# Optimization experiments

Hardware: AMD Instinct MI355X
Metric: run time of the kernel (lower is better)

Reference implementation:

```python
import jax, jax.numpy as jnp
from jax import lax
import numpy as np

IN_SIZE, H_SIZE, OUT_SIZE, SEAS = 48, 128, 48, 24
DILATIONS = (1, 2, 4, 8)  # cells 0-1 = DRNN group 0, cells 2-3 = DRNN group 1


def setup_inputs() -> dict:
    key = jax.random.key(0)
    ks = jax.random.split(key, 16)
    B, T = 256, 512
    inp = {
        'train': jax.random.uniform(ks[0], (B, T), jnp.float32, 0.5, 1.5),
        'val': jax.random.uniform(ks[1], (B, OUT_SIZE), jnp.float32, 0.5, 1.5),
        'test': jax.random.uniform(ks[2], (B, OUT_SIZE), jnp.float32, 0.5, 1.5),
        'init_lev_sm': jnp.array([0.5], jnp.float32),
        'init_seas_sm': jnp.array([0.5], jnp.float32),
        'init_seasonalities': jnp.full((SEAS,), 0.5, jnp.float32),
    }
    cin = [IN_SIZE, H_SIZE, H_SIZE, H_SIZE]
    k = 3
    for i in range(4):
        inp[f'w_ih{i}'] = jax.random.normal(ks[k], (4 * H_SIZE, cin[i]), jnp.float32) * 0.05; k += 1
        inp[f'w_hh{i}'] = jax.random.normal(ks[k], (4 * H_SIZE, H_SIZE), jnp.float32) * 0.05; k += 1
        inp[f'b_ih{i}'] = jnp.zeros((4 * H_SIZE,), jnp.float32)
        inp[f'b_hh{i}'] = jnp.zeros((4 * H_SIZE,), jnp.float32)
    inp['nl_w'] = jax.random.normal(ks[k], (H_SIZE, H_SIZE), jnp.float32) * 0.05; k += 1
    inp['nl_b'] = jnp.zeros((H_SIZE,), jnp.float32)
    inp['sc_w'] = jax.random.normal(ks[k], (OUT_SIZE, H_SIZE), jnp.float32) * 0.05; k += 1
    inp['sc_b'] = jnp.zeros((OUT_SIZE,), jnp.float32)
    return inp


def _lstm(x, w_ih, w_hh, b_ih, b_hh):
    # x: (T, N, C) -> (T, N, H); torch LSTM gate order i, f, g, o
    n, h = x.shape[1], w_hh.shape[1]

    def step(carry, xt):
        hp, cp = carry
        g = xt @ w_ih.T + hp @ w_hh.T + (b_ih + b_hh)
        i, f, gg, o = jnp.split(g, 4, axis=-1)
        c = jax.nn.sigmoid(f) * cp + jax.nn.sigmoid(i) * jnp.tanh(gg)
        hn = jax.nn.sigmoid(o) * jnp.tanh(c)
        return (hn, c), hn

    z = jnp.zeros((n, h), x.dtype)
    _, hs = lax.scan(step, (z, z), x)
    return hs


def _dilated_lstm(x, d, w_ih, w_hh, b_ih, b_hh):
    # DRNN dilation: fold time by d into batch, run cell, unfold
    t, b, c = x.shape
    td = -(-t // d) * d
    xp = jnp.pad(x, ((0, td - t), (0, 0), (0, 0)))
    xd = xp.reshape(td // d, d, b, c).reshape(td // d, d * b, c)
    out = _lstm(xd, w_ih, w_hh, b_ih, b_hh)
    h = out.shape[-1]
    return out.reshape(td // d, d, b, h).reshape(td, b, h)[:t]


def _series_forward(data, cells, nl_w, nl_b, sc_w, sc_b):
    # ResidualDRNN: group 0 (cells 0,1), group 1 (cells 2,3) with residual add
    x = data
    for grp in range(2):
        res = x
        for ci in (2 * grp, 2 * grp + 1):
            x = _dilated_lstm(x, DILATIONS[ci], *cells[ci])
        if grp > 0:
            x = x + res
    x = jnp.tanh(x @ nl_w.T + nl_b)
    return x @ sc_w.T + sc_b


def _esrnn(train, val, init_lev_sm, init_seas_sm, init_seasonalities, cells, nl_w, nl_b, sc_w, sc_b):
    B, T = train.shape
    lev_sm = jax.nn.sigmoid(init_lev_sm[0])
    seas_sm = jax.nn.sigmoid(init_seas_sm[0])
    s0 = jnp.exp(init_seasonalities)  # (SEAS,) shared across series
    lev0 = train[:, 0] / s0[0]  # (B,)
    # rolling buffer: at step i it holds seasonalities[i .. i+SEAS-1]
    buf0 = jnp.broadcast_to(jnp.concatenate([s0[1:], s0[:1]])[:, None], (SEAS, B))

    def step(carry, x_t):
        lev_p, buf = carry
        seas_t = buf[0]
        lev_n = lev_sm * (x_t / seas_t) + (1 - lev_sm) * lev_p
        seas_n = seas_sm * (x_t / lev_n) + (1 - seas_sm) * seas_t
        return (lev_n, jnp.concatenate([buf[1:], seas_n[None]], 0)), (lev_n, seas_n)

    _, (levs_r, seas_r) = lax.scan(step, (lev0, buf0), train[:, 1:].T)
    levs = jnp.concatenate([lev0[None], levs_r], 0).T  # (B, T)
    seas_head = jnp.broadcast_to(jnp.concatenate([s0, s0[:1]])[:, None], (SEAS + 1, B))
    seas = jnp.concatenate([seas_head, seas_r], 0).T  # (B, T+SEAS)
    if OUT_SIZE > SEAS:  # seasonality extension branch
        start = seas.shape[1] - SEAS
        seas = jnp.concatenate([seas, seas[:, start:start + OUT_SIZE - SEAS]], 1)
    W = T - IN_SIZE + 1
    Wo = T - OUT_SIZE - IN_SIZE + 1
    idx_in = jnp.arange(W)[:, None] + jnp.arange(IN_SIZE)[None, :]  # (W, IN)
    win_in = (train[:, idx_in] / seas[:, idx_in] / levs[:, IN_SIZE - 1:, None]).transpose(1, 0, 2)  # (W,B,IN)
    idx_out = jnp.arange(Wo)[:, None] + IN_SIZE + jnp.arange(OUT_SIZE)[None, :]
    win_out = (train[:, idx_out] / seas[:, idx_out] / levs[:, IN_SIZE - 1:IN_SIZE - 1 + Wo, None]).transpose(1, 0, 2)
    network_pred = _series_forward(win_in[:-OUT_SIZE], cells, nl_w, nl_b, sc_w, sc_b)  # (Wo,B,OUT)
    network_act = win_out
    net_out_all = _series_forward(win_in, cells, nl_w, nl_b, sc_w, sc_b)  # (W,B,OUT)
    hold = net_out_all[-1] * seas[:, -OUT_SIZE:] * levs[:, -1:]
    hold_out_pred = hold * (hold > 0).astype(hold.dtype)
    hold_out_act = val  # testing=False path
    hold_out_act_norm = val / seas[:, -OUT_SIZE:] / levs[:, -1:]
    return network_pred, network_act, hold_out_pred, net_out_all, hold_out_act, hold_out_act_norm


def reference(train, val, test, init_lev_sm, init_seas_sm, init_seasonalities,
              w_ih0, w_hh0, b_ih0, b_hh0, w_ih1, w_hh1, b_ih1, b_hh1,
              w_ih2, w_hh2, b_ih2, b_hh2, w_ih3, w_hh3, b_ih3, b_hh3,
              nl_w, nl_b, sc_w, sc_b):
    cells = ((w_ih0, w_hh0, b_ih0, b_hh0), (w_ih1, w_hh1, b_ih1, b_hh1),
             (w_ih2, w_hh2, b_ih2, b_hh2), (w_ih3, w_hh3, b_ih3, b_hh3))
    return _esrnn(train, val, init_lev_sm, init_seas_sm, init_seasonalities,
                  cells, nl_w, nl_b, sc_w, sc_b)
```

## Files before the change

### kernel.cpp

```cpp
#include <hip/hip_runtime.h>
#include <cstdint>
#include <cstddef>

typedef _Float16 half8 __attribute__((ext_vector_type(8)));
typedef _Float16 half4 __attribute__((ext_vector_type(4)));
typedef float floatx4 __attribute__((ext_vector_type(4)));

namespace {
constexpr int kB = 256, kT = 512, kIN = 48, kOUT = 48, kSEAS = 24, kH = 128;
constexpr int kW = kT - kIN + 1;
constexpr int kWO = kT - kOUT - kIN + 1;
constexpr int kNB = kW * kB;
constexpr int kMBLK = kNB / 16;
constexpr float kLOG2E = 1.44269504088896340736f;
}

#if __has_builtin(__builtin_amdgcn_exp2f)
#define FEXP2(x) __builtin_amdgcn_exp2f(x)
#else
#define FEXP2(x) exp2f(x)
#endif
#if __has_builtin(__builtin_amdgcn_rcpf)
#define FRCP(x) __builtin_amdgcn_rcpf(x)
#else
#define FRCP(x) (1.0f / (x))
#endif

#define LGKM_BARRIER() asm volatile("s_waitcnt lgkmcnt(0)\n\ts_barrier" ::: "memory")

__device__ __forceinline__ float fsig(float y) { return FRCP(1.0f + FEXP2(-y)); }
__device__ __forceinline__ float ftanh(float x) { return 2.0f * fsig(2.0f * kLOG2E * x) - 1.0f; }

__global__ void k_transpose(const float* __restrict__ train, float* __restrict__ trainT) {
  int t = blockIdx.x, b = threadIdx.x;
  trainT[t * kB + b] = train[b * kT + t];
}

__global__ void k_es(const float* __restrict__ trainT, const float* __restrict__ levp,
                     const float* __restrict__ seasp, const float* __restrict__ inits,
                     float* __restrict__ seas, float* __restrict__ levs) {
  __shared__ float ring[kSEAS][kB];
  int b = threadIdx.x;
  float lev_sm = fsig(levp[0] * kLOG2E);
  float seas_sm = fsig(seasp[0] * kLOG2E);
  float s00 = expf(inits[0]);
  for (int s = 0; s < kSEAS; ++s) {
    float v = expf(inits[s]);
    seas[s * kB + b] = v;
    if (s >= 1) ring[s - 1][b] = v;
  }
  ring[kSEAS - 1][b] = s00;
  seas[kSEAS * kB + b] = s00;
  float lev = trainT[b] * FRCP(s00);
  levs[b] = lev;
  int rk = 0;
  float x_nx = trainT[kB + b];
  float st_nx = ring[0][b];
  for (int k = 0; k < kT - 1; ++k) {
    float x = x_nx;
    float st = st_nx;
    if (k + 1 < kT - 1) x_nx = trainT[(k + 2) * kB + b];
    int rn = (rk + 1 == kSEAS) ? 0 : rk + 1;
    st_nx = ring[rn][b];
    float ln = lev_sm * (x * FRCP(st)) + (1.0f - lev_sm) * lev;
    float sn = seas_sm * (x * FRCP(ln)) + (1.0f - seas_sm) * st;
    ring[rk][b] = sn;
    seas[(k + kSEAS + 1) * kB + b] = sn;
    levs[(k + 1) * kB + b] = ln;
    lev = ln;
    rk = rn;
  }
  for (int j = 0; j < kOUT - kSEAS; ++j)
    seas[(kT + kSEAS + j) * kB + b] = seas[(kT + j) * kB + b];
}

__global__ void k_win_in(const float* __restrict__ trainT, const float* __restrict__ seas,
                         const float* __restrict__ levs, _Float16* __restrict__ win) {
  int w = blockIdx.x;
  int tid = threadIdx.x;
#pragma unroll
  for (int i = 0; i < 16; ++i) {
    int o = i * 256 + tid;
    int b = o >> 3;
    int j0 = (o & 7) * 8;
    half8 h;
    if (j0 < kIN) {
      float rl = FRCP(levs[(kIN - 1 + w) * kB + b]);
#pragma unroll
      for (int jj = 0; jj < 8; ++jj) {
        int j = j0 + jj;
        int t = w + j;
        float v = (j < kIN) ? trainT[t * kB + b] * FRCP(seas[t * kB + b]) * rl : 0.0f;
        h[jj] = (_Float16)v;
      }
    } else {
#pragma unroll
      for (int jj = 0; jj < 8; ++jj) h[jj] = (_Float16)0.0f;
    }
    *(half8*)(win + ((size_t)(w * kB + b)) * 64 + j0) = h;
  }
}

__global__ void k_win_out(const float* __restrict__ trainT, const float* __restrict__ seas,
                          const float* __restrict__ levs, float* __restrict__ out1) {
  int idx = blockIdx.x * 256 + threadIdx.x;
  if (idx >= kWO * kB * (kOUT / 4)) return;
  int row = idx / 12;
  int j0 = (idx - row * 12) * 4;
  int wo = row >> 8;
  int b = row & 255;
  float rl = FRCP(levs[(kIN - 1 + wo) * kB + b]);
  floatx4 v;
#pragma unroll
  for (int jj = 0; jj < 4; ++jj) {
    int t = kIN + wo + j0 + jj;
    v[jj] = trainT[t * kB + b] * FRCP(seas[t * kB + b]) * rl;
  }
  *(floatx4*)(out1 + (size_t)row * kOUT + j0) = v;
}

__device__ __forceinline__ void prep_bias_elem(const float* bih, const float* bhh, float* dst,
                                               int c) {
  int ct = c >> 4, n16 = c & 15, g = ct & 3, wv = ct >> 2;
  int row = g * 128 + wv * 16 + n16;
  float sc = (g == 2) ? 2.0f * kLOG2E : kLOG2E;
  dst[c] = (bih[row] + bhh[row]) * sc;
}

__device__ __forceinline__ void prep_frag_elem(const float* Wsrc, _Float16* dst, int KB, int Kreal,
                                               int srcld, int perm, int idx) {
  int jj = idx & 7;
  int lane = (idx >> 3) & 63;
  int kb = (idx >> 9) % KB;
  int ct = idx / (KB * 512);
  int n16 = lane & 15;
  int k = kb * 32 + ((lane >> 4) << 3) + jj;
  int row;
  float sc;
  if (perm) {
    int g = ct & 3, wv = ct >> 2;
    row = g * 128 + wv * 16 + n16;
    sc = (g == 2) ? 2.0f * kLOG2E : kLOG2E;
  } else {
    row = ct * 16 + n16;
    sc = 1.0f;
  }
  float v = (k < Kreal) ? Wsrc[row * srcld + k] * sc : 0.0f;
  dst[idx] = (_Float16)v;
}

struct PrepArgs {
  const float* bih[4];
  const float* bhh[4];
  float* biasp[4];
  const float* wih[4];
  _Float16* wihf[4];
  const float* whh[4];
  _Float16* whhf[4];
  const float* nlw;
  _Float16* nlf;
  const float* scw;
  _Float16* scf;
};

__global__ void k_prep_all(PrepArgs a) {
  int seg = blockIdx.y;
  int idx = blockIdx.x * 256 + threadIdx.x;
  if (seg < 4) {
    if (idx < 512) prep_bias_elem(a.bih[seg], a.bhh[seg], a.biasp[seg], idx);
  } else if (seg == 4) {
    if (idx < 32 * 2 * 512) prep_frag_elem(a.wih[0], a.wihf[0], 2, 48, 48, 1, idx);
  } else if (seg < 8) {
    int c = seg - 4;
    if (idx < 32 * 4 * 512) prep_frag_elem(a.wih[c], a.wihf[c], 4, 128, 128, 1, idx);
  } else if (seg < 12) {
    int c = seg - 8;
    if (idx < 32 * 4 * 512) prep_frag_elem(a.whh[c], a.whhf[c], 4, 128, 128, 1, idx);
  } else if (seg == 12) {
    if (idx < 8 * 4 * 512) prep_frag_elem(a.nlw, a.nlf, 4, 128, 128, 0, idx);
  } else {
    if (idx < 3 * 4 * 512) prep_frag_elem(a.scw, a.scf, 4, 128, 128, 0, idx);
  }
}

__global__ void k_zero_prog(int* prog) {
  int i = threadIdx.x;
  if (i < 192) prog[i] = 0;
}

template <int NT, int KB, int MODE>
__global__ __launch_bounds__(512) void k_gemm(const _Float16* __restrict__ A,
                                              const _Float16* __restrict__ A2, int Khalfs,
                                              const _Float16* __restrict__ Bfr,
                                              const float* __restrict__ bias,
                                              _Float16* __restrict__ outh,
                                              float* __restrict__ outf,
                                              float* __restrict__ outf2) {
  __shared__ _Float16 bsh[NT * KB * 512];
  int tid = threadIdx.x;
  {
    const uint4* src = (const uint4*)Bfr;
    uint4* dst = (uint4*)bsh;
    for (int i = tid; i < NT * KB * 64; i += 512) dst[i] = src[i];
  }
  __syncthreads();
  int wv = tid >> 6, lane = tid & 63;
  int mblk = blockIdx.x * 8 + wv;
  if (mblk >= kMBLK) return;
  int m = lane & 15, kq = lane >> 4;
  const _Float16* arow = A + (size_t)(mblk * 16 + m) * Khalfs + kq * 8;
  half8 af[KB];
#pragma unroll
  for (int kb = 0; kb < KB; ++kb) af[kb] = *(const half8*)(arow + kb * 32);
  if constexpr (MODE == 1) {
    const _Float16* arow2 = A2 + (size_t)(mblk * 16 + m) * Khalfs + kq * 8;
#pragma unroll
    for (int kb = 0; kb < KB; ++kb) {
      half8 a2 = *(const half8*)(arow2 + kb * 32);
      af[kb] += a2;
    }
  }
#pragma unroll
  for (int t0 = 0; t0 < NT; t0 += 2) {
    float b0 = bias[t0 * 16 + m];
    floatx4 acc0 = {b0, b0, b0, b0};
    floatx4 acc1 = {0.f, 0.f, 0.f, 0.f};
    if (t0 + 1 < NT) {
      float b1 = bias[(t0 + 1) * 16 + m];
      acc1 = (floatx4){b1, b1, b1, b1};
    }
#pragma unroll
    for (int kb = 0; kb < KB; ++kb) {
      half8 bf0 = *(const half8*)(&bsh[((t0 * KB + kb) * 64 + lane) * 8]);
      acc0 = __builtin_amdgcn_mfma_f32_16x16x32_f16(af[kb], bf0, acc0, 0, 0, 0);
      if (t0 + 1 < NT) {
        half8 bf1 = *(const half8*)(&bsh[(((t0 + 1) * KB + kb) * 64 + lane) * 8]);
        acc1 = __builtin_amdgcn_mfma_f32_16x16x32_f16(af[kb], bf1, acc1, 0, 0, 0);
      }
    }
    if constexpr (MODE == 0) {
      half4 h0 = {(_Float16)acc0[0], (_Float16)acc0[1], (_Float16)acc0[2], (_Float16)acc0[3]};
      *(half4*)(outh + (((size_t)mblk * NT + t0) * 64 + lane) * 4) = h0;
      if (t0 + 1 < NT) {
        half4 h1 = {(_Float16)acc1[0], (_Float16)acc1[1], (_Float16)acc1[2], (_Float16)acc1[3]};
        *(half4*)(outh + (((size_t)mblk * NT + (t0 + 1)) * 64 + lane) * 4) = h1;
      }
    } else if constexpr (MODE == 1) {
#pragma unroll
      for (int r = 0; r < 4; ++r) {
        int row = mblk * 16 + kq * 4 + r;
        outh[(size_t)row * kH + t0 * 16 + m] = (_Float16)ftanh(acc0[r]);
        if (t0 + 1 < NT) outh[(size_t)row * kH + (t0 + 1) * 16 + m] = (_Float16)ftanh(acc1[r]);
      }
    } else {
#pragma unroll
      for (int r = 0; r < 4; ++r) {
        int row = mblk * 16 + kq * 4 + r;
        float v0 = acc0[r];
        outf[(size_t)row * kOUT + t0 * 16 + m] = v0;
        if (row < kWO * kB) outf2[(size_t)row * kOUT + t0 * 16 + m] = v0;
        if (t0 + 1 < NT) {
          float v1 = acc1[r];
          outf[(size_t)row * kOUT + (t0 + 1) * 16 + m] = v1;
          if (row < kWO * kB) outf2[(size_t)row * kOUT + (t0 + 1) * 16 + m] = v1;
        }
      }
    }
  }
}

struct FArgs {
  const _Float16* xfr;
  const _Float16* win;
  const _Float16* wihf[4];
  const _Float16* whhf[4];
  const float* biasp[4];
  _Float16* H[4];
  int* prog;
};

__device__ __forceinline__ void wait_prog(int* p, int need, int& fenced, int* obs_sh) {
  if (need <= fenced) return;
  if (threadIdx.x == 0) {
    int v;
    while ((v = __hip_atomic_load(p, __ATOMIC_RELAXED, __HIP_MEMORY_SCOPE_AGENT)) < need)
      __builtin_amdgcn_s_sleep(16);
    *obs_sh = v;
  }
  __syncthreads();
  int v = *obs_sh;
  __builtin_amdgcn_fence(__ATOMIC_ACQUIRE, "agent");
  fenced = v;
}

template <int KXB, bool POLL, bool REL, bool XPRE>
__device__ __forceinline__ void floop(const _Float16* __restrict__ Xsrc,
                                      const _Float16* __restrict__ wihp,
                                      const _Float16* __restrict__ whhp,
                                      const float* __restrict__ bp, _Float16* __restrict__ Hout,
                                      int* progIn, int sprev, int* progOut, int d, int kd, int ib,
                                      _Float16 (*hbuf)[2048], int* obs_sh) {
  int tid = threadIdx.x;
  int wv = tid >> 6, lane = tid & 63, m = lane & 15, kq = lane >> 4;
  half8 wxf[4][KXB], whf[4][4];
#pragma unroll
  for (int g = 0; g < 4; ++g) {
    if (!XPRE) {
#pragma unroll
      for (int kb = 0; kb < KXB; ++kb)
        wxf[g][kb] = *(const half8*)(wihp + ((((wv * 4 + g) * KXB + kb) * 64 + lane) * 8));
    }
#pragma unroll
    for (int kb = 0; kb < 4; ++kb)
      whf[g][kb] = *(const half8*)(whhp + ((((wv * 4 + g) * 4 + kb) * 64 + lane) * 8));
  }
  float bg[4];
  if (!XPRE) {
#pragma unroll
    for (int g = 0; g < 4; ++g) bg[g] = bp[(wv * 4 + g) * 16 + m];
  }
  float cc[4] = {0.f, 0.f, 0.f, 0.f};
  int nsteps = (kW - kd + d - 1) / d;
  const int xstride = KXB * 32;
  int fenced = 0;
  if (POLL) wait_prog(progIn + (kd & ((1 << sprev) - 1)), (kd >> sprev) + 1, fenced, obs_sh);
  half8 hxc[KXB], hxn[KXB];
  half4 xr[4], xrn[4];
  if (XPRE) {
    int mb = kd * 16 + ib;
#pragma unroll
    for (int g = 0; g < 4; ++g)
      xr[g] = *(const half4*)(Xsrc + (((size_t)mb * 32 + (wv * 4 + g)) * 64 + lane) * 4);
  } else {
    const _Float16* xrow = Xsrc + (size_t)(kd * kB + ib * 16 + m) * xstride + kq * 8;
#pragma unroll
    for (int kb = 0; kb < KXB; ++kb) hxc[kb] = *(const half8*)(xrow + kb * 32);
  }
  for (int j = 0; j < nsteps; ++j) {
    int ph = j & 1;
    int wtn = (j + 1) * d + kd;
    bool havenext = (j + 1 < nsteps);
    if (POLL && havenext)
      wait_prog(progIn + (wtn & ((1 << sprev) - 1)), (wtn >> sprev) + 1, fenced, obs_sh);
    floatx4 acc[4];
    if (XPRE) {
#pragma unroll
      for (int g = 0; g < 4; ++g)
        acc[g] = (floatx4){(float)xr[g][0], (float)xr[g][1], (float)xr[g][2], (float)xr[g][3]};
    } else {
#pragma unroll
      for (int g = 0; g < 4; ++g) acc[g] = (floatx4){bg[g], bg[g], bg[g], bg[g]};
    }
    if (havenext) {
      if (XPRE) {
        int mb = wtn * 16 + ib;
#pragma unroll
        for (int g = 0; g < 4; ++g)
          xrn[g] = *(const half4*)(Xsrc + (((size_t)mb * 32 + (wv * 4 + g)) * 64 + lane) * 4);
      } else {
        const _Float16* xrow = Xsrc + (size_t)(wtn * kB + ib * 16 + m) * xstride + kq * 8;
#pragma unroll
        for (int kb = 0; kb < KXB; ++kb) hxn[kb] = *(const half8*)(xrow + kb * 32);
      }
    }
    if (!XPRE) {
#pragma unroll
      for (int kb = 0; kb < KXB; ++kb)
#pragma unroll
        for (int g = 0; g < 4; ++g)
          acc[g] = __builtin_amdgcn_mfma_f32_16x16x32_f16(hxc[kb], wxf[g][kb], acc[g], 0, 0, 0);
    }
    if (j > 0) {
#pragma unroll
      for (int kb = 0; kb < 4; ++kb) {
        int gran = (kb * 4 + kq) ^ m;
        half8 a = *(const half8*)(&hbuf[ph ^ 1][m * 128 + gran * 8]);
#pragma unroll
        for (int g = 0; g < 4; ++g)
          acc[g] = __builtin_amdgcn_mfma_f32_16x16x32_f16(a, whf[g][kb], acc[g], 0, 0, 0);
      }
    }
    _Float16 hv[4];
#pragma unroll
    for (int r = 0; r < 4; ++r) {
      float ea = FEXP2(-acc[0][r]);
      float ef = FEXP2(-acc[1][r]);
      float eb = FEXP2(-acc[2][r]);
      float eo = FEXP2(-acc[3][r]);
      float fv = FRCP(1.0f + ef);
      float it = (1.0f - eb) * FRCP((1.0f + ea) * (1.0f + eb));
      cc[r] = fv * cc[r] + it;
      float ed = FEXP2(cc[r] * (-2.0f * kLOG2E));
      float hvf = (1.0f - ed) * FRCP((1.0f + eo) * (1.0f + ed));
      hv[r] = (_Float16)hvf;
      int brow = kq * 4 + r;
      int hu = wv * 16 + m;
      int gran = (hu >> 3) ^ brow;
      hbuf[ph][brow * 128 + gran * 8 + (hu & 7)] = hv[r];
    }
    LGKM_BARRIER();
    {
      int hu = wv * 16 + m;
      size_t rb = (size_t)((j * d + kd) * kB + ib * 16 + kq * 4);
#pragma unroll
      for (int r = 0; r < 4; ++r) Hout[(rb + r) * kH + hu] = hv[r];
    }
    if (REL && (((j & 7) == 7) || (j + 1 == nsteps))) {
      __syncthreads();
      if (tid == 0)
        __hip_atomic_store(progOut, j + 1, __ATOMIC_RELEASE, __HIP_MEMORY_SCOPE_AGENT);
    }
    if (XPRE) {
#pragma unroll
      for (int g = 0; g < 4; ++g) xr[g] = xrn[g];
    } else {
#pragma unroll
      for (int kb = 0; kb < KXB; ++kb) hxc[kb] = hxn[kb];
    }
  }
}

__global__ __launch_bounds__(512) void k_fused(FArgs a) {
  __shared__ _Float16 hbuf[2][2048];
  __shared__ int obs_sh;
  int w = blockIdx.x;
  int cell, d, kd, ib;
  if (w < 16) {
    cell = 0; d = 1; kd = 0; ib = w;
  } else if (w < 48) {
    cell = 1; d = 2; kd = (w - 16) >> 4; ib = (w - 16) & 15;
  } else if (w < 112) {
    cell = 2; d = 4; kd = (w - 48) >> 4; ib = (w - 48) & 15;
  } else {
    cell = 3; d = 8; kd = (w - 112) >> 4; ib = (w - 112) & 15;
  }
  _Float16* Hout = a.H[cell];
  int* progOut = a.prog + (cell * 16 + ib) * 4 + kd;
  int* progIn = (cell > 0) ? a.prog + ((cell - 1) * 16 + ib) * 4 : nullptr;
  int sprev = (cell == 2) ? 1 : ((cell == 3) ? 2 : 0);
  if (cell == 0)
    floop<2, false, true, true>(a.xfr, nullptr, a.whhf[0], nullptr, Hout, nullptr, 0, progOut,
                                d, kd, ib, hbuf, &obs_sh);
  else if (cell < 3)
    floop<4, true, true, false>(a.H[cell - 1], a.wihf[cell], a.whhf[cell], a.biasp[cell], Hout,
                                progIn, sprev, progOut, d, kd, ib, hbuf, &obs_sh);
  else
    floop<4, true, false, false>(a.H[2], a.wihf[3], a.whhf[3], a.biasp[3], Hout, progIn, sprev,
                                 progOut, d, kd, ib, hbuf, &obs_sh);
}

__global__ void k_tail(const float* __restrict__ out3, const float* __restrict__ val,
                       const float* __restrict__ seas, const float* __restrict__ levs,
                       float* __restrict__ out2, float* __restrict__ out4,
                       float* __restrict__ out5) {
  int idx = blockIdx.x * 256 + threadIdx.x;
  int b = idx / kOUT, j = idx % kOUT;
  float s = seas[(kT + j) * kB + b];
  float L = levs[(kT - 1) * kB + b];
  float net = out3[(size_t)(kW - 1) * kB * kOUT + idx];
  float hp = net * s * L;
  out2[idx] = hp > 0.0f ? hp : 0.0f;
  float v = val[idx];
  out4[idx] = v;
  out5[idx] = v / s / L;
}

extern "C" void kernel_launch(void* const* d_in, const int* in_sizes, int n_in, void* d_out,
                              int out_size, void* d_ws, size_t ws_size, hipStream_t stream) {
  const float* train = (const float*)d_in[0];
  const float* val = (const float*)d_in[1];
  const float* levp = (const float*)d_in[3];
  const float* seasp = (const float*)d_in[4];
  const float* inits = (const float*)d_in[5];
  const float* w_ih[4] = {(const float*)d_in[6], (const float*)d_in[10], (const float*)d_in[14],
                          (const float*)d_in[18]};
  const float* w_hh[4] = {(const float*)d_in[7], (const float*)d_in[11], (const float*)d_in[15],
                          (const float*)d_in[19]};
  const float* b_ih[4] = {(const float*)d_in[8], (const float*)d_in[12], (const float*)d_in[16],
                          (const float*)d_in[20]};
  const float* b_hh[4] = {(const float*)d_in[9], (const float*)d_in[13], (const float*)d_in[17],
                          (const float*)d_in[21]};
  const float* nl_w = (const float*)d_in[22];
  const float* nl_b = (const float*)d_in[23];
  const float* sc_w = (const float*)d_in[24];
  const float* sc_b = (const float*)d_in[25];

  char* wsb = (char*)d_ws;
  size_t off = 0;
  auto alloc = [&](size_t bytes) -> void* {
    void* p = wsb + off;
    off = (off + bytes + 255) & ~(size_t)255;
    return p;
  };
  float* trainT = (float*)alloc((size_t)kT * kB * 4);
  float* seas = (float*)alloc((size_t)560 * kB * 4);
  float* levs = (float*)alloc((size_t)kT * kB * 4);
  _Float16* win = (_Float16*)alloc((size_t)kNB * 64 * 2);
  _Float16* Xfr = (_Float16*)alloc((size_t)kMBLK * 32 * 64 * 4 * 2);
  _Float16* Hc[4];
  for (int c = 0; c < 4; ++c) Hc[c] = (_Float16*)alloc((size_t)kNB * kH * 2);
  float* biasp[4];
  for (int c = 0; c < 4; ++c) biasp[c] = (float*)alloc(512 * 4);
  _Float16* wihf[4];
  wihf[0] = (_Float16*)alloc((size_t)32 * 2 * 512 * 2);
  for (int c = 1; c < 4; ++c) wihf[c] = (_Float16*)alloc((size_t)32 * 4 * 512 * 2);
  _Float16* whhf[4];
  for (int c = 0; c < 4; ++c) whhf[c] = (_Float16*)alloc((size_t)32 * 4 * 512 * 2);
  _Float16* nlf = (_Float16*)alloc((size_t)8 * 4 * 512 * 2);
  _Float16* scf = (_Float16*)alloc((size_t)3 * 4 * 512 * 2);
  int* prog = (int*)alloc(192 * 4);
  _Float16* U = Xfr;

  float* out0 = (float*)d_out;
  float* out1 = out0 + (size_t)kWO * kB * kOUT;
  float* out2 = out1 + (size_t)kWO * kB * kOUT;
  float* out3 = out2 + (size_t)kB * kOUT;
  float* out4 = out3 + (size_t)kW * kB * kOUT;
  float* out5 = out4 + (size_t)kB * kOUT;

  k_transpose<<<kT, kB, 0, stream>>>(train, trainT);
  k_es<<<1, kB, 0, stream>>>(trainT, levp, seasp, inits, seas, levs);
  k_win_in<<<kW, kB, 0, stream>>>(trainT, seas, levs, win);
  k_win_out<<<(kWO * kB * 12 + 255) / 256, 256, 0, stream>>>(trainT, seas, levs, out1);

  PrepArgs pa;
  for (int c = 0; c < 4; ++c) {
    pa.bih[c] = b_ih[c]; pa.bhh[c] = b_hh[c]; pa.biasp[c] = biasp[c];
    pa.wih[c] = w_ih[c]; pa.wihf[c] = wihf[c];
    pa.whh[c] = w_hh[c]; pa.whhf[c] = whhf[c];
  }
  pa.nlw = nl_w; pa.nlf = nlf; pa.scw = sc_w; pa.scf = scf;
  k_prep_all<<<dim3(256, 14), 256, 0, stream>>>(pa);
  k_zero_prog<<<1, 256, 0, stream>>>(prog);

  const int GG = kMBLK / 8;
  k_gemm<32, 2, 0><<<GG, 512, 0, stream>>>(win, nullptr, 64, wihf[0], biasp[0], Xfr, nullptr,
                                           nullptr);

  FArgs fa;
  fa.xfr = Xfr;
  fa.win = win;
  for (int c = 0; c < 4; ++c) {
    fa.wihf[c] = wihf[c]; fa.whhf[c] = whhf[c]; fa.biasp[c] = biasp[c]; fa.H[c] = Hc[c];
  }
  fa.prog = prog;
  void* kp[1] = {(void*)&fa};
  hipLaunchCooperativeKernel((void*)k_fused, dim3(240), dim3(512), kp, 0, stream);

  k_gemm<8, 4, 1><<<GG, 512, 0, stream>>>(Hc[3], Hc[1], 128, nlf, nl_b, U, nullptr, nullptr);
  k_gemm<3, 4, 2><<<GG, 512, 0, stream>>>(U, nullptr, 128, scf, sc_b, nullptr, out3, out0);
  k_tail<<<48, 256, 0, stream>>>(out3, val, seas, levs, out2, out4, out5);
}
```

Measured before the change: 752.4 us.

## Overlap cell-0 input projection with recurrence via partner blocks in fused kernel

Removes the standalone GEMM that precomputed cell 0's input projection (Xfr) and instead adds 16 partner blocks to the cooperative fused kernel that compute it on the fly. The partners publish per-chunk progress flags, cell-0 blocks now poll them, and the partners throttle themselves to stay a bounded distance ahead of the recurrence. The aim is to hide the projection GEMM's time behind the latency-bound LSTM recurrence. The cost is extra polling and synchronisation in cell 0's critical loop, plus more blocks in the cooperative launch.

```diff
diff --git a/kernel.cpp b/kernel.cpp
--- a/kernel.cpp
+++ b/kernel.cpp
@@ -184,8 +184,7 @@
 }
 
 __global__ void k_zero_prog(int* prog) {
-  int i = threadIdx.x;
-  if (i < 192) prog[i] = 0;
+  prog[threadIdx.x] = 0;
 }
 
 template <int NT, int KB, int MODE>
@@ -238,14 +237,7 @@
         acc1 = __builtin_amdgcn_mfma_f32_16x16x32_f16(af[kb], bf1, acc1, 0, 0, 0);
       }
     }
-    if constexpr (MODE == 0) {
-      half4 h0 = {(_Float16)acc0[0], (_Float16)acc0[1], (_Float16)acc0[2], (_Float16)acc0[3]};
-      *(half4*)(outh + (((size_t)mblk * NT + t0) * 64 + lane) * 4) = h0;
-      if (t0 + 1 < NT) {
-        half4 h1 = {(_Float16)acc1[0], (_Float16)acc1[1], (_Float16)acc1[2], (_Float16)acc1[3]};
-        *(half4*)(outh + (((size_t)mblk * NT + (t0 + 1)) * 64 + lane) * 4) = h1;
-      }
-    } else if constexpr (MODE == 1) {
+    if constexpr (MODE == 1) {
 #pragma unroll
       for (int r = 0; r < 4; ++r) {
         int row = mblk * 16 + kq * 4 + r;
@@ -270,7 +262,7 @@
 }
 
 struct FArgs {
-  const _Float16* xfr;
+  _Float16* xfr;
   const _Float16* win;
   const _Float16* wihf[4];
   const _Float16* whhf[4];
@@ -291,6 +283,56 @@
   int v = *obs_sh;
   __builtin_amdgcn_fence(__ATOMIC_ACQUIRE, "agent");
   fenced = v;
+}
+
+__device__ void partner_loop(const _Float16* __restrict__ win,
+                             const _Float16* __restrict__ wihf0,
+                             const float* __restrict__ bp, _Float16* __restrict__ Xfr,
+                             int* prog0, int* hprog, int ib) {
+  int tid = threadIdx.x, wv = tid >> 6, lane = tid & 63, m = lane & 15, kq = lane >> 4;
+  half8 wxf[4][2];
+  float bg[4];
+#pragma unroll
+  for (int g = 0; g < 4; ++g) {
+#pragma unroll
+    for (int kb = 0; kb < 2; ++kb)
+      wxf[g][kb] = *(const half8*)(wihf0 + ((((wv * 4 + g) * 2 + kb) * 64 + lane) * 8));
+    bg[g] = bp[(wv * 4 + g) * 16 + m];
+  }
+  const int AHEAD = 24;
+  for (int c = 0; c * 8 < kW; ++c) {
+    int needp = c * 8 - AHEAD;
+    if (needp > 0) {
+      if (tid == 0) {
+        while (__hip_atomic_load(prog0, __ATOMIC_RELAXED, __HIP_MEMORY_SCOPE_AGENT) < needp)
+          __builtin_amdgcn_s_sleep(32);
+      }
+      __syncthreads();
+    }
+#pragma unroll 1
+    for (int tt = 0; tt < 8; ++tt) {
+      int t = c * 8 + tt;
+      if (t >= kW) break;
+      int mb = t * 16 + ib;
+      const _Float16* arow = win + (size_t)(mb * 16 + m) * 64 + kq * 8;
+      half8 af0 = *(const half8*)(arow);
+      half8 af1 = *(const half8*)(arow + 32);
+#pragma unroll
+      for (int g = 0; g < 4; ++g) {
+        floatx4 acc = {bg[g], bg[g], bg[g], bg[g]};
+        acc = __builtin_amdgcn_mfma_f32_16x16x32_f16(af0, wxf[g][0], acc, 0, 0, 0);
+        acc = __builtin_amdgcn_mfma_f32_16x16x32_f16(af1, wxf[g][1], acc, 0, 0, 0);
+        half4 h = {(_Float16)acc[0], (_Float16)acc[1], (_Float16)acc[2], (_Float16)acc[3]};
+        *(half4*)(Xfr + (((size_t)mb * 32 + (wv * 4 + g)) * 64 + lane) * 4) = h;
+      }
+    }
+    __syncthreads();
+    if (tid == 0) {
+      int done = c * 8 + 8;
+      if (done > kW) done = kW;
+      __hip_atomic_store(hprog, done, __ATOMIC_RELEASE, __HIP_MEMORY_SCOPE_AGENT);
+    }
+  }
 }
 
 template <int KXB, bool POLL, bool REL, bool XPRE>
@@ -424,6 +466,12 @@
   __shared__ _Float16 hbuf[2][2048];
   __shared__ int obs_sh;
   int w = blockIdx.x;
+  if (w >= 240) {
+    int ib = w - 240;
+    partner_loop(a.win, a.wihf[0], a.biasp[0], a.xfr, a.prog + (0 * 16 + ib) * 4 + 0,
+                 a.prog + 192 + ib, ib);
+    return;
+  }
   int cell, d, kd, ib;
   if (w < 16) {
     cell = 0; d = 1; kd = 0; ib = w;
@@ -436,11 +484,11 @@
   }
   _Float16* Hout = a.H[cell];
   int* progOut = a.prog + (cell * 16 + ib) * 4 + kd;
-  int* progIn = (cell > 0) ? a.prog + ((cell - 1) * 16 + ib) * 4 : nullptr;
+  int* progIn = (cell > 0) ? a.prog + ((cell - 1) * 16 + ib) * 4 : a.prog + 192 + ib;
   int sprev = (cell == 2) ? 1 : ((cell == 3) ? 2 : 0);
   if (cell == 0)
-    floop<2, false, true, true>(a.xfr, nullptr, a.whhf[0], nullptr, Hout, nullptr, 0, progOut,
-                                d, kd, ib, hbuf, &obs_sh);
+    floop<2, true, true, true>(a.xfr, nullptr, a.whhf[0], nullptr, Hout, progIn, 0, progOut,
+                               d, kd, ib, hbuf, &obs_sh);
   else if (cell < 3)
     floop<4, true, true, false>(a.H[cell - 1], a.wihf[cell], a.whhf[cell], a.biasp[cell], Hout,
                                 progIn, sprev, progOut, d, kd, ib, hbuf, &obs_sh);
@@ -508,7 +556,7 @@
   for (int c = 0; c < 4; ++c) whhf[c] = (_Float16*)alloc((size_t)32 * 4 * 512 * 2);
   _Float16* nlf = (_Float16*)alloc((size_t)8 * 4 * 512 * 2);
   _Float16* scf = (_Float16*)alloc((size_t)3 * 4 * 512 * 2);
-  int* prog = (int*)alloc(192 * 4);
+  int* prog = (int*)alloc(256 * 4);
   _Float16* U = Xfr;
 
   float* out0 = (float*)d_out;
@@ -533,10 +581,6 @@
   k_prep_all<<<dim3(256, 14), 256, 0, stream>>>(pa);
   k_zero_prog<<<1, 256, 0, stream>>>(prog);
 
-  const int GG = kMBLK / 8;
-  k_gemm<32, 2, 0><<<GG, 512, 0, stream>>>(win, nullptr, 64, wihf[0], biasp[0], Xfr, nullptr,
-                                           nullptr);
-
   FArgs fa;
   fa.xfr = Xfr;
   fa.win = win;
@@ -545,8 +589,9 @@
   }
   fa.prog = prog;
   void* kp[1] = {(void*)&fa};
-  hipLaunchCooperativeKernel((void*)k_fused, dim3(240), dim3(512), kp, 0, stream);
-
+  hipLaunchCooperativeKernel((void*)k_fused, dim3(256), dim3(512), kp, 0, stream);
+
+  const int GG = kMBLK / 8;
   k_gemm<8, 4, 1><<<GG, 512, 0, stream>>>(Hc[3], Hc[1], 128, nlf, nl_b, U, nullptr, nullptr);
   k_gemm<3, 4, 2><<<GG, 512, 0, stream>>>(U, nullptr, 128, scf, sc_b, nullptr, out3, out0);
   k_tail<<<48, 256, 0, stream>>>(out3, val, seas, levs, out2, out4, out5);
```

Result: slower. 975.8 us (+29.7%).
